# Kernel tuning notes

Hardware: AMD Instinct MI355X
Metric: run time of the kernel (lower is better)

Reference implementation:

```python
import jax, jax.numpy as jnp
import numpy as np

D_MODEL = 512
N_HEADS = 8
D_FF = 2048
EPS = 1e-6


def layer_norm(x, g, b):
    mu = jnp.mean(x, axis=-1, keepdims=True)
    var = jnp.mean(jnp.square(x - mu), axis=-1, keepdims=True)
    return (x - mu) * jax.lax.rsqrt(var + EPS) * g + b


def setup_inputs() -> dict:
    key = jax.random.key(0)
    ks = jax.random.split(key, 6)
    B, S = 64, 500
    x = jax.random.normal(ks[0], (B, S, D_MODEL), dtype=jnp.float32)
    ln1_g = jnp.ones((D_MODEL,), jnp.float32)
    ln1_b = jnp.zeros((D_MODEL,), jnp.float32)
    ln2_g = jnp.ones((D_MODEL,), jnp.float32)
    ln2_b = jnp.zeros((D_MODEL,), jnp.float32)
    W1 = jax.random.normal(ks[1], (D_MODEL, D_FF), jnp.float32) * (1.0 / np.sqrt(D_MODEL))
    b1 = jnp.zeros((D_FF,), jnp.float32)
    W2 = jax.random.normal(ks[2], (D_FF, D_MODEL), jnp.float32) * (1.0 / np.sqrt(D_FF))
    b2 = jnp.zeros((D_MODEL,), jnp.float32)
    return {"x": x, "ln1_g": ln1_g, "ln1_b": ln1_b, "ln2_g": ln2_g, "ln2_b": ln2_b,
            "W1": W1, "b1": b1, "W2": W2, "b2": b2}


def causal_attention(h):
    # h: [B, S, D]; q=k=v=h (no projections in this module)
    B, S, D = h.shape
    Hd = D // N_HEADS
    qkv = h.reshape(B, S, N_HEADS, Hd).transpose(0, 2, 1, 3)  # [B, H, S, Hd]
    w = jnp.einsum('bhsd,bhtd->bhst', qkv, qkv) / jnp.sqrt(jnp.float32(Hd))
    mask = jnp.tril(jnp.ones((S, S), dtype=bool))
    w = jnp.where(mask, w, jnp.finfo(w.dtype).min)
    w = jax.nn.softmax(w, axis=-1)
    out = jnp.einsum('bhst,bhtd->bhsd', w, qkv)  # [B, H, S, Hd]
    return out.transpose(0, 2, 1, 3).reshape(B, S, D)


def reference(x, ln1_g, ln1_b, ln2_g, ln2_b, W1, b1, W2, b2):
    # Pre-LN block, but residuals attach to the post-LN activations (faithful to source).
    h = layer_norm(x, ln1_g, ln1_b)
    h = h + causal_attention(h)
    h2 = layer_norm(h, ln2_g, ln2_b)
    ff = jnp.maximum(h2 @ W1 + b1, 0.0) @ W2 + b2
    return h2 + ff
```

## Files before the change

### kernel.cpp

```cpp
#include <hip/hip_runtime.h>
#include <hip/hip_bf16.h>

#define D_MODEL 512
#define N_HEADS 8
#define HDIM 64
#define D_FF 2048
#define BATCH 64
#define SEQ 500
#define MROWS (BATCH * SEQ)

typedef __attribute__((ext_vector_type(8))) short bhalf8;
typedef __attribute__((ext_vector_type(4))) float floatx4;

#define AS_GLOBAL __attribute__((address_space(1)))
#define AS_LDS __attribute__((address_space(3)))

__device__ __forceinline__ void glds16(const void* g, void* l) {
  __builtin_amdgcn_global_load_lds((const AS_GLOBAL unsigned int*)g,
                                   (AS_LDS unsigned int*)l, 16, 0, 0);
}

__device__ __forceinline__ unsigned short f2bf(float f) {
  __hip_bfloat16 b = __float2bfloat16(f);
  return *reinterpret_cast<unsigned short*>(&b);
}

template <int MODE>
__global__ __launch_bounds__(256) void ln_kernel(const void* __restrict__ xin,
                                                 const float* __restrict__ g,
                                                 const float* __restrict__ b,
                                                 float* __restrict__ yf,
                                                 __hip_bfloat16* __restrict__ yb) {
  int row = blockIdx.x;
  int t = threadIdx.x;
  float v0, v1;
  if constexpr (MODE == 0) {
    float2 v = ((const float2*)xin)[(size_t)row * 256 + t];
    v0 = v.x; v1 = v.y;
  } else {
    __hip_bfloat162 bv = ((const __hip_bfloat162*)xin)[(size_t)row * 256 + t];
    v0 = __bfloat162float(bv.x); v1 = __bfloat162float(bv.y);
  }
  float s = v0 + v1;
  float sq = v0 * v0 + v1 * v1;
#pragma unroll
  for (int off = 32; off > 0; off >>= 1) {
    s += __shfl_down(s, off, 64);
    sq += __shfl_down(sq, off, 64);
  }
  __shared__ float red[8];
  if ((t & 63) == 0) {
    red[(t >> 6) * 2] = s;
    red[(t >> 6) * 2 + 1] = sq;
  }
  __syncthreads();
  s = red[0] + red[2] + red[4] + red[6];
  sq = red[1] + red[3] + red[5] + red[7];
  float mean = s * (1.0f / 512.0f);
  float var = sq * (1.0f / 512.0f) - mean * mean;
  float r = rsqrtf(var + 1e-6f);
  float2 gg = ((const float2*)g)[t];
  float2 bb = ((const float2*)b)[t];
  float y0 = (v0 - mean) * r * gg.x + bb.x;
  float y1 = (v1 - mean) * r * gg.y + bb.y;
  if constexpr (MODE == 1)
    ((float2*)yf)[(size_t)row * 256 + t] = make_float2(y0, y1);
  __hip_bfloat162 bv2;
  bv2.x = __float2bfloat16(y0);
  bv2.y = __float2bfloat16(y1);
  ((__hip_bfloat162*)yb)[(size_t)row * 256 + t] = bv2;
}

__global__ __launch_bounds__(256) void transpose_bf16(const float* __restrict__ W,
                                                      __hip_bfloat16* __restrict__ Wt,
                                                      int K, int N) {
  __shared__ float tile[32][33];
  int n0 = blockIdx.x * 32, k0 = blockIdx.y * 32;
  int tx = threadIdx.x, ty = threadIdx.y;
#pragma unroll
  for (int j = 0; j < 32; j += 8)
    tile[ty + j][tx] = W[(size_t)(k0 + ty + j) * N + n0 + tx];
  __syncthreads();
#pragma unroll
  for (int j = 0; j < 32; j += 8)
    Wt[(size_t)(n0 + ty + j) * K + k0 + tx] = __float2bfloat16(tile[tx][ty + j]);
}

__device__ __forceinline__ void attn_tile_step(int jq, int kt, int fr, int kg,
                                               const char* Kb, const char* Vb,
                                               char* Pw, bhalf8 (&qf)[2][2],
                                               floatx4 (&O)[2][4], float (&l)[2][4]) {
  int roff = 32 * jq - 64 * kt;
  bool domask = (jq <= 2 * kt + 1);
#pragma unroll
  for (int mr = 0; mr < 2; ++mr) {
    floatx4 S[4];
#pragma unroll
    for (int nc = 0; nc < 4; ++nc) S[nc] = (floatx4){0.f, 0.f, 0.f, 0.f};
    __builtin_amdgcn_s_setprio(1);
#pragma unroll
    for (int kk = 0; kk < 2; ++kk) {
#pragma unroll
      for (int nc = 0; nc < 4; ++nc) {
        bhalf8 kf = *(const bhalf8*)(Kb + (nc * 16 + fr) * 128 +
                                     (((kk * 4 + kg) ^ (fr & 7)) << 4));
        S[nc] = __builtin_amdgcn_mfma_f32_16x16x32_bf16(qf[mr][kk], kf, S[nc], 0, 0, 0);
      }
    }
    __builtin_amdgcn_s_setprio(0);
    if (domask) {
#pragma unroll
      for (int nc = 0; nc < 4; ++nc)
#pragma unroll
        for (int j = 0; j < 4; ++j)
          if (nc * 16 + fr > roff + mr * 16 + kg * 4 + j) S[nc][j] = -INFINITY;
    }
    float p[4][4], rs[4];
#pragma unroll
    for (int j = 0; j < 4; ++j) rs[j] = 0.f;
#pragma unroll
    for (int nc = 0; nc < 4; ++nc)
#pragma unroll
      for (int j = 0; j < 4; ++j) {
        p[nc][j] = __expf(S[nc][j] * 0.125f - 66.0f);
        rs[j] += p[nc][j];
      }
#pragma unroll
    for (int off = 1; off < 16; off <<= 1)
#pragma unroll
      for (int j = 0; j < 4; ++j) rs[j] += __shfl_xor(rs[j], off, 64);
#pragma unroll
    for (int j = 0; j < 4; ++j) l[mr][j] += rs[j];
#pragma unroll
    for (int nc = 0; nc < 4; ++nc)
#pragma unroll
      for (int j = 0; j < 4; ++j)
        *(unsigned short*)(Pw + ((kg * 4 + j) * 72 + nc * 16 + fr) * 2) = f2bf(p[nc][j]);
    __builtin_amdgcn_s_setprio(1);
#pragma unroll
    for (int kk = 0; kk < 2; ++kk) {
      bhalf8 pf = *(const bhalf8*)(Pw + fr * 144 + kk * 64 + kg * 16);
#pragma unroll
      for (int nc = 0; nc < 4; ++nc) {
        bhalf8 vf = *(const bhalf8*)(Vb + (nc * 16 + fr) * 144 + kk * 64 + kg * 16);
        O[mr][nc] = __builtin_amdgcn_mfma_f32_16x16x32_bf16(pf, vf, O[mr][nc], 0, 0, 0);
      }
    }
    __builtin_amdgcn_s_setprio(0);
  }
}

__global__ __launch_bounds__(512) void attn_fold(const __hip_bfloat16* __restrict__ hbp,
                                                 __hip_bfloat16* __restrict__ hres) {
  __shared__ unsigned short Ks[2][64 * 64];
  __shared__ unsigned short Vt[2][64 * 72];
  __shared__ unsigned short Ps[8][16 * 72];

  int blk = blockIdx.x;
  int b = blk >> 3, hd = blk & 7;
  int tid = threadIdx.x;
  int w = tid >> 6, lane = tid & 63;
  int fr = lane & 15, kg = lane >> 4;

  const unsigned short* hb = (const unsigned short*)hbp;
  size_t bbase = (size_t)b * SEQ * D_MODEL + hd * HDIM;

  int jH = 15 - w, jL = w;
  bhalf8 qH[2][2], qL[2][2];
#pragma unroll
  for (int mr = 0; mr < 2; ++mr) {
    int rH = 32 * jH + mr * 16 + fr;
    if (rH >= SEQ) rH = SEQ - 1;
    int rL = 32 * jL + mr * 16 + fr;
#pragma unroll
    for (int kk = 0; kk < 2; ++kk) {
      qH[mr][kk] = *(const bhalf8*)(hb + bbase + (size_t)rH * D_MODEL + kk * 32 + kg * 8);
      qL[mr][kk] = *(const bhalf8*)(hb + bbase + (size_t)rL * D_MODEL + kk * 32 + kg * 8);
    }
  }

  floatx4 OH[2][4], OL[2][4];
  float lHs[2][4], lLs[2][4];
#pragma unroll
  for (int mr = 0; mr < 2; ++mr)
#pragma unroll
    for (int nc = 0; nc < 4; ++nc) {
      OH[mr][nc] = (floatx4){0.f, 0.f, 0.f, 0.f};
      OL[mr][nc] = (floatx4){0.f, 0.f, 0.f, 0.f};
    }
#pragma unroll
  for (int mr = 0; mr < 2; ++mr)
#pragma unroll
    for (int j = 0; j < 4; ++j) { lHs[mr][j] = 0.f; lLs[mr][j] = 0.f; }

  int krow = w * 8 + (lane >> 3);
  int scb = (lane & 7) ^ (lane >> 3);

  {
    glds16(hb + bbase + (size_t)krow * D_MODEL + scb * 8, (char*)Ks[0] + w * 1024);
    bhalf8 v0 = *(const bhalf8*)(hb + bbase + (size_t)lane * D_MODEL + w * 8);
#pragma unroll
    for (int i = 0; i < 8; ++i) Vt[0][(w * 8 + i) * 72 + lane] = (unsigned short)v0[i];
  }
  __syncthreads();

  for (int kt = 0; kt < 8; ++kt) {
    int cur = kt & 1;
    bhalf8 vnext;
    if (kt < 7) {
      int sr = (kt + 1) * 64 + krow;
      if (sr >= SEQ) sr = SEQ - 1;
      glds16(hb + bbase + (size_t)sr * D_MODEL + scb * 8, (char*)Ks[cur ^ 1] + w * 1024);
      int vr = (kt + 1) * 64 + lane;
      if (vr >= SEQ) vr = SEQ - 1;
      vnext = *(const bhalf8*)(hb + bbase + (size_t)vr * D_MODEL + w * 8);
    }

    const char* Kb = (const char*)Ks[cur];
    const char* Vb = (const char*)Vt[cur];
    char* Pw = (char*)Ps[w];
    if (jH >= 2 * kt) attn_tile_step(jH, kt, fr, kg, Kb, Vb, Pw, qH, OH, lHs);
    if (jL >= 2 * kt) attn_tile_step(jL, kt, fr, kg, Kb, Vb, Pw, qL, OL, lLs);

    if (kt < 7) {
#pragma unroll
      for (int i = 0; i < 8; ++i)
        Vt[cur ^ 1][(w * 8 + i) * 72 + lane] = (unsigned short)vnext[i];
    }
    __syncthreads();
  }

#pragma unroll
  for (int mr = 0; mr < 2; ++mr)
#pragma unroll
    for (int j = 0; j < 4; ++j) {
      int qH_row = 32 * jH + mr * 16 + kg * 4 + j;
      if (qH_row < SEQ) {
        float inv = 1.0f / lHs[mr][j];
        size_t ro = bbase + (size_t)qH_row * D_MODEL;
#pragma unroll
        for (int nc = 0; nc < 4; ++nc) {
          size_t idx = ro + nc * 16 + fr;
          float hv = __bfloat162float(hbp[idx]);
          hres[idx] = __float2bfloat16(hv + OH[mr][nc][j] * inv);
        }
      }
      int qL_row = 32 * jL + mr * 16 + kg * 4 + j;
      {
        float inv = 1.0f / lLs[mr][j];
        size_t ro = bbase + (size_t)qL_row * D_MODEL;
#pragma unroll
        for (int nc = 0; nc < 4; ++nc) {
          size_t idx = ro + nc * 16 + fr;
          float hv = __bfloat162float(hbp[idx]);
          hres[idx] = __float2bfloat16(hv + OL[mr][nc][j] * inv);
        }
      }
    }
}

template <int EPI>
__global__ __launch_bounds__(512, 2) void gemm4b(const unsigned short* __restrict__ A,
                                                 const unsigned short* __restrict__ Bt,
                                                 const float* __restrict__ bias,
                                                 float* __restrict__ outf,
                                                 __hip_bfloat16* __restrict__ outb,
                                                 int M, int N, int K, int gx) {
  __shared__ __align__(16) char smem[4 * 32768];

  int nwg = gridDim.x;
  int bid = blockIdx.x;
  int q = nwg >> 3, r = nwg & 7;
  int xcd = bid & 7, lo = bid >> 3;
  int wg = (xcd < r ? xcd * (q + 1) : r * (q + 1) + (xcd - r) * q) + lo;
  int by = wg / gx, bx = wg % gx;
  int m0 = by * 256, n0 = bx * 256;

  int tid = threadIdx.x;
  int w = tid >> 6, lane = tid & 63;
  int wm = w >> 2, wn = w & 3;
  int fr = lane & 15, kg = lane >> 4;

  int srow = lane >> 2;
  int sswz = ((lane & 3) ^ ((lane >> 3) & 3)) * 8;
  const unsigned short* Ag0 = A + (size_t)(m0 + w * 16 + srow) * K + sswz;
  const unsigned short* Ag1 = A + (size_t)(m0 + 128 + w * 16 + srow) * K + sswz;
  const unsigned short* Bg0 = Bt + (size_t)(n0 + w * 16 + srow) * K + sswz;
  const unsigned short* Bg1 = Bt + (size_t)(n0 + 128 + w * 16 + srow) * K + sswz;
  int wA0 = w * 1024, wA1 = 8192 + w * 1024;
  int wB0 = 16384 + w * 1024, wB1 = 24576 + w * 1024;

  int swz16 = (kg ^ ((fr >> 1) & 3)) * 16;
  int aoff = wm * 8192 + fr * 64 + swz16;
  int boff = 16384 + wn * 4096 + fr * 64 + swz16;

  floatx4 acc[8][4];
#pragma unroll
  for (int i = 0; i < 8; ++i)
#pragma unroll
    for (int j = 0; j < 4; ++j) acc[i][j] = (floatx4){0.f, 0.f, 0.f, 0.f};

  int nt = K >> 5;

#define STAGE_A(t, buf)                              \
  {                                                  \
    char* d = smem + (buf) * 32768;                  \
    glds16(Ag0 + (size_t)(t) * 32, d + wA0);         \
    glds16(Ag1 + (size_t)(t) * 32, d + wA1);         \
  }
#define STAGE_B(t, buf)                              \
  {                                                  \
    char* d = smem + (buf) * 32768;                  \
    glds16(Bg0 + (size_t)(t) * 32, d + wB0);         \
    glds16(Bg1 + (size_t)(t) * 32, d + wB1);         \
  }

  STAGE_A(0, 0); STAGE_B(0, 0);
  STAGE_A(1, 1); STAGE_B(1, 1);
  STAGE_A(2, 2); STAGE_B(2, 2);
  asm volatile("s_waitcnt vmcnt(8)" ::: "memory");
  __builtin_amdgcn_s_barrier();

  for (int t = 0; t < nt; ++t) {
    const char* bufp = smem + (t & 3) * 32768;
    int sb = (t + 3) & 3;
    bool s3 = (t + 3) < nt, s2 = (t + 2) < nt, s1 = (t + 1) < nt;
    bhalf8 afr[4], bfr[4];

    if (s3) STAGE_A(t + 3, sb);
#pragma unroll
    for (int nn = 0; nn < 4; ++nn)
      bfr[nn] = *(const bhalf8*)(bufp + boff + nn * 1024);
#pragma unroll
    for (int mm = 0; mm < 4; ++mm)
      afr[mm] = *(const bhalf8*)(bufp + aoff + mm * 1024);
    __builtin_amdgcn_s_barrier();
    __builtin_amdgcn_s_setprio(1);
#pragma unroll
    for (int mm = 0; mm < 4; ++mm)
#pragma unroll
      for (int nn = 0; nn < 4; ++nn)
        acc[mm][nn] =
            __builtin_amdgcn_mfma_f32_16x16x32_bf16(afr[mm], bfr[nn], acc[mm][nn], 0, 0, 0);
    __builtin_amdgcn_s_setprio(0);
    __builtin_amdgcn_s_barrier();

    if (s3) STAGE_B(t + 3, sb);
#pragma unroll
    for (int mm = 0; mm < 4; ++mm)
      afr[mm] = *(const bhalf8*)(bufp + aoff + (4 + mm) * 1024);
    __builtin_amdgcn_s_barrier();
    __builtin_amdgcn_s_setprio(1);
#pragma unroll
    for (int mm = 0; mm < 4; ++mm)
#pragma unroll
      for (int nn = 0; nn < 4; ++nn)
        acc[4 + mm][nn] =
            __builtin_amdgcn_mfma_f32_16x16x32_bf16(afr[mm], bfr[nn], acc[4 + mm][nn], 0, 0, 0);
    __builtin_amdgcn_s_setprio(0);
    if (s3)
      asm volatile("s_waitcnt vmcnt(8)" ::: "memory");
    else if (s2)
      asm volatile("s_waitcnt vmcnt(4)" ::: "memory");
    else if (s1)
      asm volatile("s_waitcnt vmcnt(0)" ::: "memory");
    __builtin_amdgcn_s_barrier();
  }
#undef STAGE_A
#undef STAGE_B

  int grow_base = m0 + wm * 128 + kg * 4;
  int gcol_base = n0 + wn * 64 + fr;
#pragma unroll
  for (int mm = 0; mm < 8; ++mm) {
#pragma unroll
    for (int nn = 0; nn < 4; ++nn) {
      int gc = gcol_base + nn * 16;
      float bi = bias[gc];
#pragma unroll
      for (int j = 0; j < 4; ++j) {
        int gr = grow_base + mm * 16 + j;
        float v = acc[mm][nn][j] + bi;
        if (EPI == 1) {
          v = v > 0.f ? v : 0.f;
          outb[(size_t)gr * N + gc] = __float2bfloat16(v);
        } else {
          size_t idx = (size_t)gr * N + gc;
          outf[idx] = outf[idx] + v;
        }
      }
    }
  }
}

extern "C" void kernel_launch(void* const* d_in, const int* in_sizes, int n_in,
                              void* d_out, int out_size, void* d_ws, size_t ws_size,
                              hipStream_t stream) {
  const float* x = (const float*)d_in[0];
  const float* ln1g = (const float*)d_in[1];
  const float* ln1b = (const float*)d_in[2];
  const float* ln2g = (const float*)d_in[3];
  const float* ln2b = (const float*)d_in[4];
  const float* W1 = (const float*)d_in[5];
  const float* b1 = (const float*)d_in[6];
  const float* W2 = (const float*)d_in[7];
  const float* b2 = (const float*)d_in[8];
  float* out = (float*)d_out;

  char* ws = (char*)d_ws;
  __hip_bfloat16* h2b = (__hip_bfloat16*)ws;
  __hip_bfloat16* hb = (__hip_bfloat16*)(ws + 65536000);
  __hip_bfloat16* hresb = (__hip_bfloat16*)(ws + 98304000);
  __hip_bfloat16* u = (__hip_bfloat16*)(ws + 98304000);
  __hip_bfloat16* W1t = (__hip_bfloat16*)(ws + 229376000);
  __hip_bfloat16* W2t = (__hip_bfloat16*)(ws + 231473152);

  transpose_bf16<<<dim3(D_FF / 32, D_MODEL / 32), dim3(32, 8), 0, stream>>>(
      W1, W1t, D_MODEL, D_FF);
  transpose_bf16<<<dim3(D_MODEL / 32, D_FF / 32), dim3(32, 8), 0, stream>>>(
      W2, W2t, D_FF, D_MODEL);

  ln_kernel<0><<<MROWS, 256, 0, stream>>>(x, ln1g, ln1b, nullptr, hb);

  attn_fold<<<BATCH * N_HEADS, 512, 0, stream>>>(hb, hresb);

  ln_kernel<1><<<MROWS, 256, 0, stream>>>(hresb, ln2g, ln2b, out, h2b);

  gemm4b<1><<<(MROWS / 256) * (D_FF / 256), 512, 0, stream>>>(
      (const unsigned short*)h2b, (const unsigned short*)W1t, b1, nullptr, u,
      MROWS, D_FF, D_MODEL, D_FF / 256);
  gemm4b<2><<<(MROWS / 256) * (D_MODEL / 256), 512, 0, stream>>>(
      (const unsigned short*)u, (const unsigned short*)W2t, b2, out, nullptr,
      MROWS, D_MODEL, D_FF, D_MODEL / 256);
}
```

Baseline: 330.2 us.

## Replace 4-stage BK32 GEMM pipeline with double-buffered BK64 tiles

```diff
diff --git a/kernel.cpp b/kernel.cpp
--- a/kernel.cpp
+++ b/kernel.cpp
@@ -260,13 +260,13 @@
 }
 
 template <int EPI>
-__global__ __launch_bounds__(512, 2) void gemm4b(const unsigned short* __restrict__ A,
-                                                 const unsigned short* __restrict__ Bt,
-                                                 const float* __restrict__ bias,
-                                                 float* __restrict__ outf,
-                                                 __hip_bfloat16* __restrict__ outb,
-                                                 int M, int N, int K, int gx) {
-  __shared__ __align__(16) char smem[4 * 32768];
+__global__ __launch_bounds__(512) void gemmbk64(const unsigned short* __restrict__ A,
+                                                const unsigned short* __restrict__ Bt,
+                                                const float* __restrict__ bias,
+                                                float* __restrict__ outf,
+                                                __hip_bfloat16* __restrict__ outb,
+                                                int M, int N, int K, int gx) {
+  __shared__ __align__(16) char smem[2 * 65536];
 
   int nwg = gridDim.x;
   int bid = blockIdx.x;
@@ -281,18 +281,21 @@
   int wm = w >> 2, wn = w & 3;
   int fr = lane & 15, kg = lane >> 4;
 
-  int srow = lane >> 2;
-  int sswz = ((lane & 3) ^ ((lane >> 3) & 3)) * 8;
-  const unsigned short* Ag0 = A + (size_t)(m0 + w * 16 + srow) * K + sswz;
-  const unsigned short* Ag1 = A + (size_t)(m0 + 128 + w * 16 + srow) * K + sswz;
-  const unsigned short* Bg0 = Bt + (size_t)(n0 + w * 16 + srow) * K + sswz;
-  const unsigned short* Bg1 = Bt + (size_t)(n0 + 128 + w * 16 + srow) * K + sswz;
-  int wA0 = w * 1024, wA1 = 8192 + w * 1024;
-  int wB0 = 16384 + w * 1024, wB1 = 24576 + w * 1024;
-
-  int swz16 = (kg ^ ((fr >> 1) & 3)) * 16;
-  int aoff = wm * 8192 + fr * 64 + swz16;
-  int boff = 16384 + wn * 4096 + fr * 64 + swz16;
+  int srow = lane >> 3;
+  int scol = ((lane & 7) ^ srow) * 8;
+  const unsigned short* Ag0 = A + (size_t)(m0 + (w)*8 + srow) * K + scol;
+  const unsigned short* Ag1 = A + (size_t)(m0 + (w + 8) * 8 + srow) * K + scol;
+  const unsigned short* Ag2 = A + (size_t)(m0 + (w + 16) * 8 + srow) * K + scol;
+  const unsigned short* Ag3 = A + (size_t)(m0 + (w + 24) * 8 + srow) * K + scol;
+  const unsigned short* Bg0 = Bt + (size_t)(n0 + (w)*8 + srow) * K + scol;
+  const unsigned short* Bg1 = Bt + (size_t)(n0 + (w + 8) * 8 + srow) * K + scol;
+  const unsigned short* Bg2 = Bt + (size_t)(n0 + (w + 16) * 8 + srow) * K + scol;
+  const unsigned short* Bg3 = Bt + (size_t)(n0 + (w + 24) * 8 + srow) * K + scol;
+
+  int slot0 = ((kg ^ (fr & 7)) << 4);
+  int slot1 = (((4 + kg) ^ (fr & 7)) << 4);
+  int abase = (wm * 128 + fr) * 128;
+  int bbase = 32768 + (wn * 64 + fr) * 128;
 
   floatx4 acc[8][4];
 #pragma unroll
@@ -300,74 +303,55 @@
 #pragma unroll
     for (int j = 0; j < 4; ++j) acc[i][j] = (floatx4){0.f, 0.f, 0.f, 0.f};
 
-  int nt = K >> 5;
-
-#define STAGE_A(t, buf)                              \
-  {                                                  \
-    char* d = smem + (buf) * 32768;                  \
-    glds16(Ag0 + (size_t)(t) * 32, d + wA0);         \
-    glds16(Ag1 + (size_t)(t) * 32, d + wA1);         \
-  }
-#define STAGE_B(t, buf)                              \
-  {                                                  \
-    char* d = smem + (buf) * 32768;                  \
-    glds16(Bg0 + (size_t)(t) * 32, d + wB0);         \
-    glds16(Bg1 + (size_t)(t) * 32, d + wB1);         \
-  }
-
-  STAGE_A(0, 0); STAGE_B(0, 0);
-  STAGE_A(1, 1); STAGE_B(1, 1);
-  STAGE_A(2, 2); STAGE_B(2, 2);
-  asm volatile("s_waitcnt vmcnt(8)" ::: "memory");
+  int nt = K >> 6;
+
+#define STAGE(t, buf)                                       \
+  {                                                         \
+    char* d = smem + (buf)*65536;                           \
+    glds16(Ag0 + (size_t)(t)*64, d + (w)*1024);             \
+    glds16(Ag1 + (size_t)(t)*64, d + (w + 8) * 1024);       \
+    glds16(Ag2 + (size_t)(t)*64, d + (w + 16) * 1024);      \
+    glds16(Ag3 + (size_t)(t)*64, d + (w + 24) * 1024);      \
+    glds16(Bg0 + (size_t)(t)*64, d + 32768 + (w)*1024);     \
+    glds16(Bg1 + (size_t)(t)*64, d + 32768 + (w + 8) * 1024); \
+    glds16(Bg2 + (size_t)(t)*64, d + 32768 + (w + 16) * 1024); \
+    glds16(Bg3 + (size_t)(t)*64, d + 32768 + (w + 24) * 1024); \
+  }
+
+  STAGE(0, 0);
+  asm volatile("s_waitcnt vmcnt(0)" ::: "memory");
   __builtin_amdgcn_s_barrier();
 
   for (int t = 0; t < nt; ++t) {
-    const char* bufp = smem + (t & 3) * 32768;
-    int sb = (t + 3) & 3;
-    bool s3 = (t + 3) < nt, s2 = (t + 2) < nt, s1 = (t + 1) < nt;
-    bhalf8 afr[4], bfr[4];
-
-    if (s3) STAGE_A(t + 3, sb);
-#pragma unroll
-    for (int nn = 0; nn < 4; ++nn)
-      bfr[nn] = *(const bhalf8*)(bufp + boff + nn * 1024);
-#pragma unroll
-    for (int mm = 0; mm < 4; ++mm)
-      afr[mm] = *(const bhalf8*)(bufp + aoff + mm * 1024);
-    __builtin_amdgcn_s_barrier();
+    const char* bufp = smem + (t & 1) * 65536;
+    if (t + 1 < nt) STAGE(t + 1, (t + 1) & 1);
+    __builtin_amdgcn_sched_barrier(0);
+
+    bhalf8 bfr[2][4];
+#pragma unroll
+    for (int nn = 0; nn < 4; ++nn) {
+      bfr[0][nn] = *(const bhalf8*)(bufp + bbase + nn * 2048 + slot0);
+      bfr[1][nn] = *(const bhalf8*)(bufp + bbase + nn * 2048 + slot1);
+    }
     __builtin_amdgcn_s_setprio(1);
 #pragma unroll
-    for (int mm = 0; mm < 4; ++mm)
+    for (int mm = 0; mm < 8; ++mm) {
+      bhalf8 a0 = *(const bhalf8*)(bufp + abase + mm * 2048 + slot0);
 #pragma unroll
       for (int nn = 0; nn < 4; ++nn)
         acc[mm][nn] =
-            __builtin_amdgcn_mfma_f32_16x16x32_bf16(afr[mm], bfr[nn], acc[mm][nn], 0, 0, 0);
+            __builtin_amdgcn_mfma_f32_16x16x32_bf16(a0, bfr[0][nn], acc[mm][nn], 0, 0, 0);
+      bhalf8 a1 = *(const bhalf8*)(bufp + abase + mm * 2048 + slot1);
+#pragma unroll
+      for (int nn = 0; nn < 4; ++nn)
+        acc[mm][nn] =
+            __builtin_amdgcn_mfma_f32_16x16x32_bf16(a1, bfr[1][nn], acc[mm][nn], 0, 0, 0);
+    }
     __builtin_amdgcn_s_setprio(0);
+    if (t + 1 < nt) asm volatile("s_waitcnt vmcnt(0)" ::: "memory");
     __builtin_amdgcn_s_barrier();
-
-    if (s3) STAGE_B(t + 3, sb);
-#pragma unroll
-    for (int mm = 0; mm < 4; ++mm)
-      afr[mm] = *(const bhalf8*)(bufp + aoff + (4 + mm) * 1024);
-    __builtin_amdgcn_s_barrier();
-    __builtin_amdgcn_s_setprio(1);
-#pragma unroll
-    for (int mm = 0; mm < 4; ++mm)
-#pragma unroll
-      for (int nn = 0; nn < 4; ++nn)
-        acc[4 + mm][nn] =
-            __builtin_amdgcn_mfma_f32_16x16x32_bf16(afr[mm], bfr[nn], acc[4 + mm][nn], 0, 0, 0);
-    __builtin_amdgcn_s_setprio(0);
-    if (s3)
-      asm volatile("s_waitcnt vmcnt(8)" ::: "memory");
-    else if (s2)
-      asm volatile("s_waitcnt vmcnt(4)" ::: "memory");
-    else if (s1)
-      asm volatile("s_waitcnt vmcnt(0)" ::: "memory");
-    __builtin_amdgcn_s_barrier();
-  }
-#undef STAGE_A
-#undef STAGE_B
+  }
+#undef STAGE
 
   int grow_base = m0 + wm * 128 + kg * 4;
   int gcol_base = n0 + wn * 64 + fr;
@@ -426,10 +410,10 @@
 
   ln_kernel<1><<<MROWS, 256, 0, stream>>>(hresb, ln2g, ln2b, out, h2b);
 
-  gemm4b<1><<<(MROWS / 256) * (D_FF / 256), 512, 0, stream>>>(
+  gemmbk64<1><<<(MROWS / 256) * (D_FF / 256), 512, 0, stream>>>(
       (const unsigned short*)h2b, (const unsigned short*)W1t, b1, nullptr, u,
       MROWS, D_FF, D_MODEL, D_FF / 256);
-  gemm4b<2><<<(MROWS / 256) * (D_MODEL / 256), 512, 0, stream>>>(
+  gemmbk64<2><<<(MROWS / 256) * (D_MODEL / 256), 512, 0, stream>>>(
       (const unsigned short*)u, (const unsigned short*)W2t, b2, out, nullptr,
       MROWS, D_MODEL, D_FF, D_MODEL / 256);
 }
```

After: 322.2 us. 2.4% less time.

## Restructure GEMM pipeline into 64-wide K steps with 8-phase staggered LDS staging

Applied to the files above, without the earlier changes.

```diff
diff --git a/kernel.cpp b/kernel.cpp
--- a/kernel.cpp
+++ b/kernel.cpp
@@ -260,13 +260,13 @@
 }
 
 template <int EPI>
-__global__ __launch_bounds__(512, 2) void gemm4b(const unsigned short* __restrict__ A,
-                                                 const unsigned short* __restrict__ Bt,
-                                                 const float* __restrict__ bias,
-                                                 float* __restrict__ outf,
-                                                 __hip_bfloat16* __restrict__ outb,
-                                                 int M, int N, int K, int gx) {
-  __shared__ __align__(16) char smem[4 * 32768];
+__global__ __launch_bounds__(512, 2) void gemm8ph(const unsigned short* __restrict__ A,
+                                                  const unsigned short* __restrict__ Bt,
+                                                  const float* __restrict__ bias,
+                                                  float* __restrict__ outf,
+                                                  __hip_bfloat16* __restrict__ outb,
+                                                  int M, int N, int K, int gx) {
+  __shared__ __align__(16) char smem[8 * 16384];
 
   int nwg = gridDim.x;
   int bid = blockIdx.x;
@@ -281,18 +281,18 @@
   int wm = w >> 2, wn = w & 3;
   int fr = lane & 15, kg = lane >> 4;
 
-  int srow = lane >> 2;
-  int sswz = ((lane & 3) ^ ((lane >> 3) & 3)) * 8;
-  const unsigned short* Ag0 = A + (size_t)(m0 + w * 16 + srow) * K + sswz;
-  const unsigned short* Ag1 = A + (size_t)(m0 + 128 + w * 16 + srow) * K + sswz;
-  const unsigned short* Bg0 = Bt + (size_t)(n0 + w * 16 + srow) * K + sswz;
-  const unsigned short* Bg1 = Bt + (size_t)(n0 + 128 + w * 16 + srow) * K + sswz;
-  int wA0 = w * 1024, wA1 = 8192 + w * 1024;
-  int wB0 = 16384 + w * 1024, wB1 = 24576 + w * 1024;
-
-  int swz16 = (kg ^ ((fr >> 1) & 3)) * 16;
-  int aoff = wm * 8192 + fr * 64 + swz16;
-  int boff = 16384 + wn * 4096 + fr * 64 + swz16;
+  int srow0 = w * 32 + (lane >> 2);
+  int srow1 = srow0 + 16;
+  int scol = ((lane & 3) ^ ((lane >> 3) & 3)) * 8;
+  const unsigned short* Ag0 = A + (size_t)(m0 + srow0) * K + scol;
+  const unsigned short* Ag1 = A + (size_t)(m0 + srow1) * K + scol;
+  const unsigned short* Bg0 = Bt + (size_t)(n0 + srow0) * K + scol;
+  const unsigned short* Bg1 = Bt + (size_t)(n0 + srow1) * K + scol;
+  int wdst = w * 2048;
+
+  int swz16 = (kg ^ ((fr >> 1) & 3)) << 4;
+  int abase = wm * 8192 + fr * 64 + swz16;
+  int bbase = wn * 4096 + fr * 64 + swz16;
 
   floatx4 acc[8][4];
 #pragma unroll
@@ -300,40 +300,36 @@
 #pragma unroll
     for (int j = 0; j < 4; ++j) acc[i][j] = (floatx4){0.f, 0.f, 0.f, 0.f};
 
-  int nt = K >> 5;
-
-#define STAGE_A(t, buf)                              \
-  {                                                  \
-    char* d = smem + (buf) * 32768;                  \
-    glds16(Ag0 + (size_t)(t) * 32, d + wA0);         \
-    glds16(Ag1 + (size_t)(t) * 32, d + wA1);         \
-  }
-#define STAGE_B(t, buf)                              \
-  {                                                  \
-    char* d = smem + (buf) * 32768;                  \
-    glds16(Bg0 + (size_t)(t) * 32, d + wB0);         \
-    glds16(Bg1 + (size_t)(t) * 32, d + wB1);         \
-  }
-
-  STAGE_A(0, 0); STAGE_B(0, 0);
-  STAGE_A(1, 1); STAGE_B(1, 1);
-  STAGE_A(2, 2); STAGE_B(2, 2);
+  int nt = K >> 6;
+
+#define STAGE(P0, P1, t, kh, par, isB)                                      \
+  {                                                                         \
+    char* d = smem + (((par) * 4 + (kh) * 2 + (isB)) * 16384) + wdst;       \
+    glds16(P0 + (size_t)(t) * 64 + (kh) * 32, d);                           \
+    glds16(P1 + (size_t)(t) * 64 + (kh) * 32, d + 1024);                    \
+  }
+
+  STAGE(Ag0, Ag1, 0, 0, 0, 0); STAGE(Bg0, Bg1, 0, 0, 0, 1);
+  STAGE(Ag0, Ag1, 0, 1, 0, 0); STAGE(Bg0, Bg1, 0, 1, 0, 1);
+  STAGE(Ag0, Ag1, 1, 0, 1, 0); STAGE(Bg0, Bg1, 1, 0, 1, 1);
   asm volatile("s_waitcnt vmcnt(8)" ::: "memory");
   __builtin_amdgcn_s_barrier();
 
   for (int t = 0; t < nt; ++t) {
-    const char* bufp = smem + (t & 3) * 32768;
-    int sb = (t + 3) & 3;
-    bool s3 = (t + 3) < nt, s2 = (t + 2) < nt, s1 = (t + 1) < nt;
-    bhalf8 afr[4], bfr[4];
-
-    if (s3) STAGE_A(t + 3, sb);
-#pragma unroll
-    for (int nn = 0; nn < 4; ++nn)
-      bfr[nn] = *(const bhalf8*)(bufp + boff + nn * 1024);
-#pragma unroll
-    for (int mm = 0; mm < 4; ++mm)
-      afr[mm] = *(const bhalf8*)(bufp + aoff + mm * 1024);
+    int par = t & 1, parn = par ^ 1;
+    const char* As0 = smem + (par * 4 + 0) * 16384;
+    const char* Bs0 = smem + (par * 4 + 1) * 16384;
+    const char* As1 = smem + (par * 4 + 2) * 16384;
+    const char* Bs1 = smem + (par * 4 + 3) * 16384;
+    bool g1 = (t + 1) < nt, g2 = (t + 2) < nt;
+    bool tail = (t + 2) >= nt;
+    bhalf8 av[4], bv[4];
+
+#pragma unroll
+    for (int nn = 0; nn < 4; ++nn) bv[nn] = *(const bhalf8*)(Bs0 + bbase + nn * 1024);
+#pragma unroll
+    for (int mm = 0; mm < 4; ++mm) av[mm] = *(const bhalf8*)(As0 + abase + mm * 1024);
+    if (g1) STAGE(Ag0, Ag1, t + 1, 1, parn, 0);
     __builtin_amdgcn_s_barrier();
     __builtin_amdgcn_s_setprio(1);
 #pragma unroll
@@ -341,14 +337,14 @@
 #pragma unroll
       for (int nn = 0; nn < 4; ++nn)
         acc[mm][nn] =
-            __builtin_amdgcn_mfma_f32_16x16x32_bf16(afr[mm], bfr[nn], acc[mm][nn], 0, 0, 0);
-    __builtin_amdgcn_s_setprio(0);
-    __builtin_amdgcn_s_barrier();
-
-    if (s3) STAGE_B(t + 3, sb);
-#pragma unroll
-    for (int mm = 0; mm < 4; ++mm)
-      afr[mm] = *(const bhalf8*)(bufp + aoff + (4 + mm) * 1024);
+            __builtin_amdgcn_mfma_f32_16x16x32_bf16(av[mm], bv[nn], acc[mm][nn], 0, 0, 0);
+    __builtin_amdgcn_s_setprio(0);
+    __builtin_amdgcn_s_barrier();
+
+#pragma unroll
+    for (int mm = 0; mm < 4; ++mm)
+      av[mm] = *(const bhalf8*)(As0 + abase + (4 + mm) * 1024);
+    if (g1) STAGE(Bg0, Bg1, t + 1, 1, parn, 1);
     __builtin_amdgcn_s_barrier();
     __builtin_amdgcn_s_setprio(1);
 #pragma unroll
@@ -356,18 +352,50 @@
 #pragma unroll
       for (int nn = 0; nn < 4; ++nn)
         acc[4 + mm][nn] =
-            __builtin_amdgcn_mfma_f32_16x16x32_bf16(afr[mm], bfr[nn], acc[4 + mm][nn], 0, 0, 0);
-    __builtin_amdgcn_s_setprio(0);
-    if (s3)
+            __builtin_amdgcn_mfma_f32_16x16x32_bf16(av[mm], bv[nn], acc[4 + mm][nn], 0, 0, 0);
+    __builtin_amdgcn_s_setprio(0);
+    if (!tail)
       asm volatile("s_waitcnt vmcnt(8)" ::: "memory");
-    else if (s2)
-      asm volatile("s_waitcnt vmcnt(4)" ::: "memory");
-    else if (s1)
+    else
       asm volatile("s_waitcnt vmcnt(0)" ::: "memory");
     __builtin_amdgcn_s_barrier();
-  }
-#undef STAGE_A
-#undef STAGE_B
+
+#pragma unroll
+    for (int nn = 0; nn < 4; ++nn) bv[nn] = *(const bhalf8*)(Bs1 + bbase + nn * 1024);
+#pragma unroll
+    for (int mm = 0; mm < 4; ++mm) av[mm] = *(const bhalf8*)(As1 + abase + mm * 1024);
+    if (g2) STAGE(Ag0, Ag1, t + 2, 0, par, 0);
+    __builtin_amdgcn_s_barrier();
+    __builtin_amdgcn_s_setprio(1);
+#pragma unroll
+    for (int mm = 0; mm < 4; ++mm)
+#pragma unroll
+      for (int nn = 0; nn < 4; ++nn)
+        acc[mm][nn] =
+            __builtin_amdgcn_mfma_f32_16x16x32_bf16(av[mm], bv[nn], acc[mm][nn], 0, 0, 0);
+    __builtin_amdgcn_s_setprio(0);
+    __builtin_amdgcn_s_barrier();
+
+#pragma unroll
+    for (int mm = 0; mm < 4; ++mm)
+      av[mm] = *(const bhalf8*)(As1 + abase + (4 + mm) * 1024);
+    if (g2) STAGE(Bg0, Bg1, t + 2, 0, par, 1);
+    __builtin_amdgcn_s_barrier();
+    __builtin_amdgcn_s_setprio(1);
+#pragma unroll
+    for (int mm = 0; mm < 4; ++mm)
+#pragma unroll
+      for (int nn = 0; nn < 4; ++nn)
+        acc[4 + mm][nn] =
+            __builtin_amdgcn_mfma_f32_16x16x32_bf16(av[mm], bv[nn], acc[4 + mm][nn], 0, 0, 0);
+    __builtin_amdgcn_s_setprio(0);
+    if (!tail)
+      asm volatile("s_waitcnt vmcnt(8)" ::: "memory");
+    else
+      asm volatile("s_waitcnt vmcnt(0)" ::: "memory");
+    __builtin_amdgcn_s_barrier();
+  }
+#undef STAGE
 
   int grow_base = m0 + wm * 128 + kg * 4;
   int gcol_base = n0 + wn * 64 + fr;
@@ -426,10 +454,10 @@
 
   ln_kernel<1><<<MROWS, 256, 0, stream>>>(hresb, ln2g, ln2b, out, h2b);
 
-  gemm4b<1><<<(MROWS / 256) * (D_FF / 256), 512, 0, stream>>>(
+  gemm8ph<1><<<(MROWS / 256) * (D_FF / 256), 512, 0, stream>>>(
       (const unsigned short*)h2b, (const unsigned short*)W1t, b1, nullptr, u,
       MROWS, D_FF, D_MODEL, D_FF / 256);
-  gemm4b<2><<<(MROWS / 256) * (D_MODEL / 256), 512, 0, stream>>>(
+  gemm8ph<2><<<(MROWS / 256) * (D_MODEL / 256), 512, 0, stream>>>(
       (const unsigned short*)u, (const unsigned short*)W2t, b2, out, nullptr,
       MROWS, D_MODEL, D_FF, D_MODEL / 256);
 }
```

Result: faster. 311.9 us (-5.5%).
